# Optimization experiments

Hardware: AMD Instinct MI355X
Metric: run time of the kernel (lower is better)

## Reference

```python
import jax, jax.numpy as jnp
import numpy as np

N, E, F = 32768, 131072, 32

# (l_in, l_edge, l_out, op_type) for each of the 12 active paths; index = row of W
PATHS = [
    (0, 0, 0, 'prod'), (0, 1, 1, 'prod'), (0, 2, 2, 'prod'),
    (1, 0, 1, 'prod'), (2, 0, 2, 'prod'),
    (1, 1, 0, 'dot'), (1, 1, 1, 'cross'), (1, 1, 2, 'outer'),
    (2, 1, 1, 'mat_vec'), (1, 2, 1, 'vec_mat'),
    (2, 2, 0, 'double_dot'), (2, 2, 2, 'mat_mul_sym'),
]


def setup_inputs() -> dict:
    key = jax.random.key(0)
    ks = jax.random.split(key, 8)
    return {
        'h0': jax.random.normal(ks[0], (N, F), jnp.float32),
        'h1': jax.random.normal(ks[1], (N, 3, F), jnp.float32),
        'h2': jax.random.normal(ks[2], (N, 3, 3, F), jnp.float32),
        'g0': jax.random.normal(ks[3], (E, F), jnp.float32),
        'g1': jax.random.normal(ks[4], (E, 3, F), jnp.float32),
        'g2': jax.random.normal(ks[5], (E, 3, 3, F), jnp.float32),
        'W': jax.random.normal(ks[6], (len(PATHS), F, F), jnp.float32) * (F ** -0.5),
        'src': jax.random.randint(ks[7], (E,), 0, N, jnp.int32).astype(jnp.int64),
    }


def _leibniz(h0, h1, h2, g0, g1, g2, W, src):
    inv_sqrt_f = h0.shape[-1] ** -0.5
    # gather source-node features once per l
    h = {0: h0[src], 1: h1[src], 2: h2[src]}
    g = {0: g0, 1: g1, 2: g2}
    eye = jnp.eye(3, dtype=h0.dtype)[None, :, :, None]  # [1,3,3,1]
    msgs = {0: [], 1: [], 2: []}
    for p, (li, le, lo, op) in enumerate(PATHS):
        # nn.Linear(F,F,bias=False): y = x @ W^T, applied on last (feature) axis
        ht = jnp.einsum('...f,gf->...g', h[li], W[p])
        geom = g[le]
        if op == 'prod':
            if li == 0 and le == 0:
                res = ht * geom
            elif li == 0 and le == 1:
                res = ht[:, None, :] * geom
            elif li == 0 and le == 2:
                res = ht[:, None, None, :] * geom
            elif li == 1 and le == 0:
                res = ht * geom[:, None, :]
            else:  # li == 2, le == 0
                res = ht * geom[:, None, None, :]
        elif op == 'dot':
            res = jnp.sum(ht * geom, axis=1)
        elif op == 'cross':
            res = jnp.cross(ht, geom, axisa=1, axisb=1, axisc=1)
        elif op == 'outer':
            outer = ht[:, :, None, :] * geom[:, None, :, :]  # [E,3,3,F]
            trace = jnp.einsum('eiif->ef', outer)
            res = outer - (1.0 / 3.0) * trace[:, None, None, :] * eye
        elif op == 'mat_vec':
            res = jnp.einsum('eijf,ejf->eif', ht, geom)
        elif op == 'vec_mat':
            res = jnp.einsum('eif,eijf->ejf', ht, geom)
        elif op == 'double_dot':
            res = jnp.sum(ht * geom, axis=(1, 2))
        else:  # mat_mul_sym
            raw = jnp.einsum('eikf,ekjf->eijf', ht, geom)
            sym = 0.5 * (raw + jnp.swapaxes(raw, 1, 2))
            trace = jnp.einsum('eiif->ef', sym)
            res = sym - (1.0 / 3.0) * trace[:, None, None, :] * eye
        msgs[lo].append(res * inv_sqrt_f)
    return tuple(sum(msgs[l]) for l in (0, 1, 2))


def reference(h0, h1, h2, g0, g1, g2, W, src):
    return _leibniz(h0, h1, h2, g0, g1, g2, W, src)
```

## Files before the change

kernel.cpp:

```cpp
#include <hip/hip_runtime.h>

typedef float f32x4 __attribute__((ext_vector_type(4)));
typedef __bf16 bf16x8 __attribute__((ext_vector_type(8)));

constexpr float INV_SQRT_F = 0.17677669529663687f;

__device__ __forceinline__ f32x4 mfma16(bf16x8 a, bf16x8 b) {
  const f32x4 z = {0.f, 0.f, 0.f, 0.f};
  return __builtin_amdgcn_mfma_f32_16x16x32_bf16(a, b, z, 0, 0, 0);
}

__device__ __forceinline__ bf16x8 load_frag8(const float* __restrict__ p) {
  f32x4 u = *reinterpret_cast<const f32x4*>(p);
  f32x4 v = *reinterpret_cast<const f32x4*>(p + 4);
  bf16x8 r;
  r[0] = (__bf16)u[0]; r[1] = (__bf16)u[1]; r[2] = (__bf16)u[2]; r[3] = (__bf16)u[3];
  r[4] = (__bf16)v[0]; r[5] = (__bf16)v[1]; r[6] = (__bf16)v[2]; r[7] = (__bf16)v[3];
  return r;
}

__device__ __forceinline__ f32x4 ntload4(const float* __restrict__ p) {
  return __builtin_nontemporal_load(reinterpret_cast<const f32x4*>(p));
}
__device__ __forceinline__ void ntstore4(float* __restrict__ p, f32x4 v) {
  __builtin_nontemporal_store(v, reinterpret_cast<f32x4*>(p));
}

__global__ __launch_bounds__(256, 2)
void leibniz_fused(const float* __restrict__ h0, const float* __restrict__ h1,
                   const float* __restrict__ h2, const float* __restrict__ g0,
                   const float* __restrict__ g1, const float* __restrict__ g2,
                   const float* __restrict__ Wg, const int* __restrict__ src,
                   float* __restrict__ out, int E)
{
  __shared__ bf16x8 wlds[12 * 2 * 4 * 16];

  for (int c = threadIdx.x; c < 12 * 2 * 4 * 16; c += 256) {
    const int gl = c & 15;
    const int qq = (c >> 4) & 3;
    const int hf = (c >> 6) & 1;
    const int p  = c >> 7;
    const float* wp = Wg + (p * 32 + hf * 16 + gl) * 32 + qq * 8;
    bf16x8 f;
#pragma unroll
    for (int j = 0; j < 8; ++j) f[j] = (__bf16)(wp[j] * INV_SQRT_F);
    wlds[c] = f;
  }
  __syncthreads();

  const int lane = threadIdx.x & 63;
  const int wid  = threadIdx.x >> 6;
  const int eidx = lane & 15;
  const int q    = lane >> 4;
  int e0 = (blockIdx.x * 4 + wid) * 16;
  if (e0 > E - 16) e0 = E - 16;

  const int node = src[e0 + eidx];

  const int e   = e0 + eidx;
  const int col = q * 4;
  const float* g0p = g0 + e * 32 + col;
  const float* g1p = g1 + (long long)e * 96 + col;
  const float* g2p = g2 + (long long)e * 288 + col;

  f32x4 gv0[2];
  gv0[0] = ntload4(g0p);
  gv0[1] = ntload4(g0p + 16);
  f32x4 gv1[3][2];
#pragma unroll
  for (int s = 0; s < 3; ++s) {
    gv1[s][0] = ntload4(g1p + s * 32);
    gv1[s][1] = ntload4(g1p + s * 32 + 16);
  }

  const int k0 = q * 8;
  const bf16x8 b0 = load_frag8(h0 + node * 32 + k0);
  bf16x8 b1[3];
#pragma unroll
  for (int s = 0; s < 3; ++s) b1[s] = load_frag8(h1 + node * 96 + s * 32 + k0);
  bf16x8 b2[9];
#pragma unroll
  for (int s = 0; s < 9; ++s) b2[s] = load_frag8(h2 + node * 288 + s * 32 + k0);

  const f32x4 z4 = {0.f, 0.f, 0.f, 0.f};
  f32x4 acc0[2] = {z4, z4};
  f32x4 acc1[3][2];
  f32x4 acc2[9][2];
#pragma unroll
  for (int s = 0; s < 3; ++s) { acc1[s][0] = z4; acc1[s][1] = z4; }
#pragma unroll
  for (int s = 0; s < 9; ++s) { acc2[s][0] = z4; acc2[s][1] = z4; }

#define WFRAG(P, H) (wlds[(((P) * 2 + (H)) * 4 + q) * 16 + eidx])

#pragma unroll
  for (int h = 0; h < 2; ++h) {
    acc0[h] += mfma16(WFRAG(0, h), b0) * gv0[h];
    const bf16x8 w3 = WFRAG(3, h);
#pragma unroll
    for (int s = 0; s < 3; ++s) acc1[s][h] += mfma16(w3, b1[s]) * gv0[h];
    const bf16x8 w4 = WFRAG(4, h);
#pragma unroll
    for (int s = 0; s < 9; ++s) acc2[s][h] += mfma16(w4, b2[s]) * gv0[h];
  }

  f32x4 gkA[3][2];
#pragma unroll
  for (int j = 0; j < 3; ++j) {
    gkA[j][0] = ntload4(g2p + j * 32);
    gkA[j][1] = ntload4(g2p + j * 32 + 16);
  }

#pragma unroll
  for (int h = 0; h < 2; ++h) {
    {
      const f32x4 t = mfma16(WFRAG(1, h), b0);
#pragma unroll
      for (int s = 0; s < 3; ++s) acc1[s][h] += t * gv1[s][h];
    }
    {
      const bf16x8 w5 = WFRAG(5, h);
#pragma unroll
      for (int s = 0; s < 3; ++s) acc0[h] += mfma16(w5, b1[s]) * gv1[s][h];
    }
    {
      const bf16x8 w6 = WFRAG(6, h);
      const f32x4 c0 = mfma16(w6, b1[0]);
      const f32x4 c1 = mfma16(w6, b1[1]);
      const f32x4 c2 = mfma16(w6, b1[2]);
      acc1[0][h] += c1 * gv1[2][h] - c2 * gv1[1][h];
      acc1[1][h] += c2 * gv1[0][h] - c0 * gv1[2][h];
      acc1[2][h] += c0 * gv1[1][h] - c1 * gv1[0][h];
    }
    {
      const bf16x8 w7 = WFRAG(7, h);
      const f32x4 o0 = mfma16(w7, b1[0]);
      const f32x4 o1 = mfma16(w7, b1[1]);
      const f32x4 o2 = mfma16(w7, b1[2]);
      const f32x4 tr3 = (o0 * gv1[0][h] + o1 * gv1[1][h] + o2 * gv1[2][h]) * (1.f / 3.f);
      acc2[0][h] += o0 * gv1[0][h] - tr3;
      acc2[1][h] += o0 * gv1[1][h];
      acc2[2][h] += o0 * gv1[2][h];
      acc2[3][h] += o1 * gv1[0][h];
      acc2[4][h] += o1 * gv1[1][h] - tr3;
      acc2[5][h] += o1 * gv1[2][h];
      acc2[6][h] += o2 * gv1[0][h];
      acc2[7][h] += o2 * gv1[1][h];
      acc2[8][h] += o2 * gv1[2][h] - tr3;
    }
    {
      const bf16x8 w8 = WFRAG(8, h);
#pragma unroll
      for (int i = 0; i < 3; ++i)
#pragma unroll
        for (int j = 0; j < 3; ++j)
          acc1[i][h] += mfma16(w8, b2[i * 3 + j]) * gv1[j][h];
    }
  }

  f32x4 gkB[3][2];
#pragma unroll
  for (int j = 0; j < 3; ++j) {
    gkB[j][0] = ntload4(g2p + (3 + j) * 32);
    gkB[j][1] = ntload4(g2p + (3 + j) * 32 + 16);
  }

  f32x4 t2[2];
  t2[0] = mfma16(WFRAG(2, 0), b0);
  t2[1] = mfma16(WFRAG(2, 1), b0);

#define G2ROW_COMPUTE(K, GK)                                                   \
  {                                                                            \
    _Pragma("unroll")                                                          \
    for (int h = 0; h < 2; ++h) {                                              \
      _Pragma("unroll")                                                        \
      for (int j = 0; j < 3; ++j) acc2[(K) * 3 + j][h] += t2[h] * GK[j][h];    \
      {                                                                        \
        const f32x4 vk = mfma16(WFRAG(9, h), b1[(K)]);                         \
        _Pragma("unroll")                                                      \
        for (int j = 0; j < 3; ++j) acc1[j][h] += vk * GK[j][h];               \
      }                                                                        \
      {                                                                        \
        const bf16x8 w10 = WFRAG(10, h);                                       \
        _Pragma("unroll")                                                      \
        for (int j = 0; j < 3; ++j)                                            \
          acc0[h] += mfma16(w10, b2[(K) * 3 + j]) * GK[j][h];                  \
      }                                                                        \
      {                                                                        \
        const bf16x8 w11 = WFRAG(11, h);                                       \
        const f32x4 m0 = mfma16(w11, b2[0 * 3 + (K)]);                         \
        const f32x4 m1 = mfma16(w11, b2[1 * 3 + (K)]);                         \
        const f32x4 m2 = mfma16(w11, b2[2 * 3 + (K)]);                         \
        const f32x4 tk3 =                                                      \
            (m0 * GK[0][h] + m1 * GK[1][h] + m2 * GK[2][h]) * (1.f / 3.f);     \
        acc2[0][h] += m0 * GK[0][h] - tk3;                                     \
        acc2[4][h] += m1 * GK[1][h] - tk3;                                     \
        acc2[8][h] += m2 * GK[2][h] - tk3;                                     \
        const f32x4 s01 = (m0 * GK[1][h] + m1 * GK[0][h]) * 0.5f;              \
        acc2[1][h] += s01; acc2[3][h] += s01;                                  \
        const f32x4 s02 = (m0 * GK[2][h] + m2 * GK[0][h]) * 0.5f;              \
        acc2[2][h] += s02; acc2[6][h] += s02;                                  \
        const f32x4 s12 = (m1 * GK[2][h] + m2 * GK[1][h]) * 0.5f;              \
        acc2[5][h] += s12; acc2[7][h] += s12;                                  \
      }                                                                        \
    }                                                                          \
  }

  G2ROW_COMPUTE(0, gkA)

#pragma unroll
  for (int j = 0; j < 3; ++j) {
    gkA[j][0] = ntload4(g2p + (6 + j) * 32);
    gkA[j][1] = ntload4(g2p + (6 + j) * 32 + 16);
  }

  G2ROW_COMPUTE(1, gkB)
  G2ROW_COMPUTE(2, gkA)

#undef G2ROW_COMPUTE

  float* o0p = out + (long long)e * 32 + col;
  float* o1p = out + (long long)E * 32 + (long long)e * 96 + col;
  float* o2p = out + (long long)E * 128 + (long long)e * 288 + col;

  ntstore4(o0p, acc0[0]);
  ntstore4(o0p + 16, acc0[1]);
#pragma unroll
  for (int s = 0; s < 3; ++s) {
    ntstore4(o1p + s * 32, acc1[s][0]);
    ntstore4(o1p + s * 32 + 16, acc1[s][1]);
  }
#pragma unroll
  for (int s = 0; s < 9; ++s) {
    ntstore4(o2p + s * 32, acc2[s][0]);
    ntstore4(o2p + s * 32 + 16, acc2[s][1]);
  }
#undef WFRAG
}

extern "C" void kernel_launch(void* const* d_in, const int* in_sizes, int n_in,
                              void* d_out, int out_size, void* d_ws, size_t ws_size,
                              hipStream_t stream) {
  const float* h0 = (const float*)d_in[0];
  const float* h1 = (const float*)d_in[1];
  const float* h2 = (const float*)d_in[2];
  const float* g0 = (const float*)d_in[3];
  const float* g1 = (const float*)d_in[4];
  const float* g2 = (const float*)d_in[5];
  const float* Wg = (const float*)d_in[6];
  const int* src = (const int*)d_in[7];
  const int E = in_sizes[7];
  const int blocks = (E + 63) / 64;
  leibniz_fused<<<blocks, 256, 0, stream>>>(h0, h1, h2, g0, g1, g2, Wg, src,
                                            (float*)d_out, E);
}
```

Measured before the change: 126.9 us.

## Precompute per-node linear transforms into bf16 workspace, then per-edge geometry kernel

Splits the fused kernel into two kernels. The first applies all 12 path weight matrices once per node with MFMA and stores bf16 results in the workspace. The second gathers those per-node transforms for each edge and combines them with the edge geometry using only elementwise math. This removes the redundant per-edge matrix multiplies, but each edge now gathers a larger transformed feature block and there is an extra kernel launch. The original fused kernel is kept as a fallback when the workspace is too small.

After: 198.0 us. +56.1%, slower.

```diff
diff --git a/kernel.cpp b/kernel.cpp
--- a/kernel.cpp
+++ b/kernel.cpp
@@ -2,6 +2,7 @@
 
 typedef float f32x4 __attribute__((ext_vector_type(4)));
 typedef __bf16 bf16x8 __attribute__((ext_vector_type(8)));
+typedef __bf16 bf16x4 __attribute__((ext_vector_type(4)));
 
 constexpr float INV_SQRT_F = 0.17677669529663687f;
 
@@ -9,16 +10,223 @@
   const f32x4 z = {0.f, 0.f, 0.f, 0.f};
   return __builtin_amdgcn_mfma_f32_16x16x32_bf16(a, b, z, 0, 0, 0);
 }
-
-__device__ __forceinline__ bf16x8 load_frag8(const float* __restrict__ p) {
-  f32x4 u = *reinterpret_cast<const f32x4*>(p);
-  f32x4 v = *reinterpret_cast<const f32x4*>(p + 4);
+__device__ __forceinline__ f32x4 ld4(const float* p) {
+  return *reinterpret_cast<const f32x4*>(p);
+}
+__device__ __forceinline__ bf16x4 ldb4(const __bf16* p) {
+  return *reinterpret_cast<const bf16x4*>(p);
+}
+__device__ __forceinline__ f32x4 b2f4(bf16x4 v) {
+  f32x4 r;
+  r[0] = (float)v[0]; r[1] = (float)v[1]; r[2] = (float)v[2]; r[3] = (float)v[3];
+  return r;
+}
+__device__ __forceinline__ bf16x4 f2b4(f32x4 v) {
+  bf16x4 r;
+  r[0] = (__bf16)v[0]; r[1] = (__bf16)v[1]; r[2] = (__bf16)v[2]; r[3] = (__bf16)v[3];
+  return r;
+}
+__device__ __forceinline__ bf16x8 cvt_frag(f32x4 u, f32x4 v) {
   bf16x8 r;
   r[0] = (__bf16)u[0]; r[1] = (__bf16)u[1]; r[2] = (__bf16)u[2]; r[3] = (__bf16)u[3];
   r[4] = (__bf16)v[0]; r[5] = (__bf16)v[1]; r[6] = (__bf16)v[2]; r[7] = (__bf16)v[3];
   return r;
 }
 
+
+__global__ __launch_bounds__(256, 2)
+void node_transform(const float* __restrict__ h0, const float* __restrict__ h1,
+                    const float* __restrict__ h2, const float* __restrict__ Wg,
+                    __bf16* __restrict__ T, int N)
+{
+  __shared__ bf16x8 wlds[12 * 2 * 4 * 16];
+  for (int c = threadIdx.x; c < 12 * 2 * 4 * 16; c += 256) {
+    const int gl = c & 15;
+    const int qq = (c >> 4) & 3;
+    const int hf = (c >> 6) & 1;
+    const int p  = c >> 7;
+    const float* wp = Wg + (p * 32 + hf * 16 + gl) * 32 + qq * 8;
+    bf16x8 f;
+#pragma unroll
+    for (int j = 0; j < 8; ++j) f[j] = (__bf16)(wp[j] * INV_SQRT_F);
+    wlds[c] = f;
+  }
+  __syncthreads();
+
+  const int lane = threadIdx.x & 63;
+  const int wid  = threadIdx.x >> 6;
+  const int eidx = lane & 15;
+  const int q    = lane >> 4;
+  int nb = (blockIdx.x * 4 + wid) * 16;
+  if (nb > N - 16) nb = N - 16;
+  const int node = nb + eidx;
+  const int k0 = q * 8;
+
+  const float* h0p = h0 + (long long)node * 32 + k0;
+  const float* h1p = h1 + (long long)node * 96 + k0;
+  const float* h2p = h2 + (long long)node * 288 + k0;
+  f32x4 r0a = ld4(h0p), r0b = ld4(h0p + 4);
+  f32x4 r1[6];
+#pragma unroll
+  for (int s = 0; s < 3; ++s) { r1[2*s] = ld4(h1p + s*32); r1[2*s+1] = ld4(h1p + s*32 + 4); }
+  f32x4 r2[18];
+#pragma unroll
+  for (int s = 0; s < 9; ++s) { r2[2*s] = ld4(h2p + s*32); r2[2*s+1] = ld4(h2p + s*32 + 4); }
+
+  const bf16x8 b0 = cvt_frag(r0a, r0b);
+  bf16x8 b1[3];
+#pragma unroll
+  for (int s = 0; s < 3; ++s) b1[s] = cvt_frag(r1[2*s], r1[2*s+1]);
+  bf16x8 b2[9];
+#pragma unroll
+  for (int s = 0; s < 9; ++s) b2[s] = cvt_frag(r2[2*s], r2[2*s+1]);
+
+  __bf16* tn = T + (long long)node * 1728;
+
+#define WF(P, H) (wlds[(((P) * 2 + (H)) * 4 + q) * 16 + eidx])
+#define ST(OFF, V) *reinterpret_cast<bf16x4*>(tn + (OFF) + fo) = f2b4(V)
+
+  const int l1p[5] = {3, 5, 6, 7, 9};
+  const int l2p[4] = {4, 8, 10, 11};
+#pragma unroll
+  for (int h = 0; h < 2; ++h) {
+    const int fo = 16 * h + 4 * q;
+    ST(0 * 32, mfma16(WF(0, h), b0));
+    ST(1 * 32, mfma16(WF(1, h), b0));
+    ST(2 * 32, mfma16(WF(2, h), b0));
+#pragma unroll
+    for (int b = 0; b < 5; ++b)
+#pragma unroll
+      for (int s = 0; s < 3; ++s)
+        ST(96 + b * 96 + s * 32, mfma16(WF(l1p[b], h), b1[s]));
+#pragma unroll
+    for (int d = 0; d < 4; ++d)
+#pragma unroll
+      for (int ss = 0; ss < 9; ++ss)
+        ST(576 + d * 288 + ss * 32, mfma16(WF(l2p[d], h), b2[ss]));
+  }
+#undef ST
+#undef WF
+}
+
+__global__ __launch_bounds__(256, 3)
+void edge_geometry(const __bf16* __restrict__ T, const float* __restrict__ g0,
+                   const float* __restrict__ g1, const float* __restrict__ g2,
+                   const int* __restrict__ src, float* __restrict__ out, int E)
+{
+  const int i = blockIdx.x * 256 + threadIdx.x;
+  const int e = i >> 3;
+  if (e >= E) return;
+  const int fo = (i & 7) * 4;
+
+  const int node = src[e];
+  const float* gp0 = g0 + (long long)e * 32 + fo;
+  const float* gp1 = g1 + (long long)e * 96 + fo;
+  const float* gp2 = g2 + (long long)e * 288 + fo;
+  const __bf16* tn = T + (long long)node * 1728 + fo;
+
+  const f32x4 gv0 = ld4(gp0);
+  f32x4 gv1[3];
+#pragma unroll
+  for (int s = 0; s < 3; ++s) gv1[s] = ld4(gp1 + s * 32);
+  f32x4 gkA[3], gkB[3];
+#pragma unroll
+  for (int j = 0; j < 3; ++j) gkA[j] = ld4(gp2 + j * 32);
+#pragma unroll
+  for (int j = 0; j < 3; ++j) gkB[j] = ld4(gp2 + (3 + j) * 32);
+
+  f32x4 acc0 = b2f4(ldb4(tn + 0)) * gv0;
+  f32x4 acc1[3];
+#pragma unroll
+  for (int s = 0; s < 3; ++s) acc1[s] = b2f4(ldb4(tn + 96 + s * 32)) * gv0;
+  f32x4 acc2[9];
+#pragma unroll
+  for (int ss = 0; ss < 9; ++ss) acc2[ss] = b2f4(ldb4(tn + 576 + ss * 32)) * gv0;
+
+  {
+    const f32x4 h1v = b2f4(ldb4(tn + 32));
+#pragma unroll
+    for (int s = 0; s < 3; ++s) acc1[s] += h1v * gv1[s];
+  }
+#pragma unroll
+  for (int s = 0; s < 3; ++s)
+    acc0 += b2f4(ldb4(tn + 192 + s * 32)) * gv1[s];
+  {
+    f32x4 h6[3];
+#pragma unroll
+    for (int s = 0; s < 3; ++s) h6[s] = b2f4(ldb4(tn + 288 + s * 32));
+    acc1[0] += h6[1] * gv1[2] - h6[2] * gv1[1];
+    acc1[1] += h6[2] * gv1[0] - h6[0] * gv1[2];
+    acc1[2] += h6[0] * gv1[1] - h6[1] * gv1[0];
+  }
+  {
+    f32x4 h7[3];
+#pragma unroll
+    for (int s = 0; s < 3; ++s) h7[s] = b2f4(ldb4(tn + 384 + s * 32));
+    const f32x4 tr3 = (h7[0] * gv1[0] + h7[1] * gv1[1] + h7[2] * gv1[2]) * (1.f / 3.f);
+#pragma unroll
+    for (int a = 0; a < 3; ++a)
+#pragma unroll
+      for (int b = 0; b < 3; ++b) acc2[a * 3 + b] += h7[a] * gv1[b];
+    acc2[0] -= tr3; acc2[4] -= tr3; acc2[8] -= tr3;
+  }
+#pragma unroll
+  for (int a = 0; a < 3; ++a)
+#pragma unroll
+    for (int b = 0; b < 3; ++b)
+      acc1[a] += b2f4(ldb4(tn + 864 + (a * 3 + b) * 32)) * gv1[b];
+
+  const f32x4 h2v = b2f4(ldb4(tn + 64));
+  f32x4 h9[3];
+#pragma unroll
+  for (int s = 0; s < 3; ++s) h9[s] = b2f4(ldb4(tn + 480 + s * 32));
+
+#define G2ROW(K, GK)                                                           \
+  {                                                                            \
+    _Pragma("unroll")                                                          \
+    for (int j = 0; j < 3; ++j) acc2[(K) * 3 + j] += h2v * GK[j];              \
+    _Pragma("unroll")                                                          \
+    for (int j = 0; j < 3; ++j) acc1[j] += h9[(K)] * GK[j];                    \
+    _Pragma("unroll")                                                          \
+    for (int j = 0; j < 3; ++j)                                                \
+      acc0 += b2f4(ldb4(tn + 1152 + ((K) * 3 + j) * 32)) * GK[j];              \
+    {                                                                          \
+      const f32x4 m0 = b2f4(ldb4(tn + 1440 + (0 * 3 + (K)) * 32));             \
+      const f32x4 m1 = b2f4(ldb4(tn + 1440 + (1 * 3 + (K)) * 32));             \
+      const f32x4 m2 = b2f4(ldb4(tn + 1440 + (2 * 3 + (K)) * 32));             \
+      const f32x4 tk3 = (m0 * GK[0] + m1 * GK[1] + m2 * GK[2]) * (1.f / 3.f);  \
+      acc2[0] += m0 * GK[0] - tk3;                                             \
+      acc2[4] += m1 * GK[1] - tk3;                                             \
+      acc2[8] += m2 * GK[2] - tk3;                                             \
+      const f32x4 s01 = (m0 * GK[1] + m1 * GK[0]) * 0.5f;                      \
+      acc2[1] += s01; acc2[3] += s01;                                          \
+      const f32x4 s02 = (m0 * GK[2] + m2 * GK[0]) * 0.5f;                      \
+      acc2[2] += s02; acc2[6] += s02;                                          \
+      const f32x4 s12 = (m1 * GK[2] + m2 * GK[1]) * 0.5f;                      \
+      acc2[5] += s12; acc2[7] += s12;                                          \
+    }                                                                          \
+  }
+
+  G2ROW(0, gkA)
+#pragma unroll
+  for (int j = 0; j < 3; ++j) gkA[j] = ld4(gp2 + (6 + j) * 32);
+  G2ROW(1, gkB)
+  G2ROW(2, gkA)
+#undef G2ROW
+
+  float* o0p = out + (long long)e * 32 + fo;
+  float* o1p = out + (long long)E * 32 + (long long)e * 96 + fo;
+  float* o2p = out + (long long)E * 128 + (long long)e * 288 + fo;
+  *reinterpret_cast<f32x4*>(o0p) = acc0;
+#pragma unroll
+  for (int s = 0; s < 3; ++s) *reinterpret_cast<f32x4*>(o1p + s * 32) = acc1[s];
+#pragma unroll
+  for (int s = 0; s < 9; ++s) *reinterpret_cast<f32x4*>(o2p + s * 32) = acc2[s];
+}
+
+__device__ __forceinline__ bf16x8 load_frag8(const float* __restrict__ p) {
+  return cvt_frag(ld4(p), ld4(p + 4));
+}
 __device__ __forceinline__ f32x4 ntload4(const float* __restrict__ p) {
   return __builtin_nontemporal_load(reinterpret_cast<const f32x4*>(p));
 }
@@ -34,7 +242,6 @@
                    float* __restrict__ out, int E)
 {
   __shared__ bf16x8 wlds[12 * 2 * 4 * 16];
-
   for (int c = threadIdx.x; c < 12 * 2 * 4 * 16; c += 256) {
     const int gl = c & 15;
     const int qq = (c >> 4) & 3;
@@ -56,7 +263,6 @@
   if (e0 > E - 16) e0 = E - 16;
 
   const int node = src[e0 + eidx];
-
   const int e   = e0 + eidx;
   const int col = q * 4;
   const float* g0p = g0 + e * 32 + col;
@@ -64,8 +270,7 @@
   const float* g2p = g2 + (long long)e * 288 + col;
 
   f32x4 gv0[2];
-  gv0[0] = ntload4(g0p);
-  gv0[1] = ntload4(g0p + 16);
+  gv0[0] = ntload4(g0p); gv0[1] = ntload4(g0p + 16);
   f32x4 gv1[3][2];
 #pragma unroll
   for (int s = 0; s < 3; ++s) {
@@ -92,7 +297,6 @@
   for (int s = 0; s < 9; ++s) { acc2[s][0] = z4; acc2[s][1] = z4; }
 
 #define WFRAG(P, H) (wlds[(((P) * 2 + (H)) * 4 + q) * 16 + eidx])
-
 #pragma unroll
   for (int h = 0; h < 2; ++h) {
     acc0[h] += mfma16(WFRAG(0, h), b0) * gv0[h];
@@ -151,10 +355,10 @@
     {
       const bf16x8 w8 = WFRAG(8, h);
 #pragma unroll
-      for (int i = 0; i < 3; ++i)
-#pragma unroll
-        for (int j = 0; j < 3; ++j)
-          acc1[i][h] += mfma16(w8, b2[i * 3 + j]) * gv1[j][h];
+      for (int a = 0; a < 3; ++a)
+#pragma unroll
+        for (int b = 0; b < 3; ++b)
+          acc1[a][h] += mfma16(w8, b2[a * 3 + b]) * gv1[b][h];
     }
   }
 
@@ -207,22 +411,18 @@
   }
 
   G2ROW_COMPUTE(0, gkA)
-
 #pragma unroll
   for (int j = 0; j < 3; ++j) {
     gkA[j][0] = ntload4(g2p + (6 + j) * 32);
     gkA[j][1] = ntload4(g2p + (6 + j) * 32 + 16);
   }
-
   G2ROW_COMPUTE(1, gkB)
   G2ROW_COMPUTE(2, gkA)
-
 #undef G2ROW_COMPUTE
 
   float* o0p = out + (long long)e * 32 + col;
   float* o1p = out + (long long)E * 32 + (long long)e * 96 + col;
   float* o2p = out + (long long)E * 128 + (long long)e * 288 + col;
-
   ntstore4(o0p, acc0[0]);
   ntstore4(o0p + 16, acc0[1]);
 #pragma unroll
@@ -250,7 +450,16 @@
   const float* Wg = (const float*)d_in[6];
   const int* src = (const int*)d_in[7];
   const int E = in_sizes[7];
-  const int blocks = (E + 63) / 64;
-  leibniz_fused<<<blocks, 256, 0, stream>>>(h0, h1, h2, g0, g1, g2, Wg, src,
-                                            (float*)d_out, E);
-}
+  const int N = in_sizes[0] / 32;
+
+  const size_t need = (size_t)N * 1728 * 2;
+  if (ws_size >= need) {
+    __bf16* T = (__bf16*)d_ws;
+    node_transform<<<(N + 63) / 64, 256, 0, stream>>>(h0, h1, h2, Wg, T, N);
+    edge_geometry<<<(E * 8 + 255) / 256, 256, 0, stream>>>(T, g0, g1, g2, src,
+                                                           (float*)d_out, E);
+  } else {
+    leibniz_fused<<<(E + 63) / 64, 256, 0, stream>>>(h0, h1, h2, g0, g1, g2,
+                                                     Wg, src, (float*)d_out, E);
+  }
+}
```

## Add bf16 prepass for node features and split feature halves across waves

Applied to the files above, without the earlier changes.

Adds a prepass kernel that converts h0/h1/h2 and the scaled W to bf16 in workspace, so the main kernel gathers half-size node rows instead of fp32 rows it converts per edge. The main kernel now gives each wave one 16-column half of the outputs, which halves per-thread accumulators and register pressure and loads all of g2 up front. It also switches from nontemporal to regular loads and stores. The cost is an extra launch plus a full read and write pass over the node features, and each weight tile is now fetched from workspace per block.

New measurement: 141.1 us. +11.2%, slower.

```diff
diff --git a/kernel.cpp b/kernel.cpp
--- a/kernel.cpp
+++ b/kernel.cpp
@@ -2,6 +2,7 @@
 
 typedef float f32x4 __attribute__((ext_vector_type(4)));
 typedef __bf16 bf16x8 __attribute__((ext_vector_type(8)));
+typedef __bf16 bf16x4 __attribute__((ext_vector_type(4)));
 
 constexpr float INV_SQRT_F = 0.17677669529663687f;
 
@@ -9,16 +10,222 @@
   const f32x4 z = {0.f, 0.f, 0.f, 0.f};
   return __builtin_amdgcn_mfma_f32_16x16x32_bf16(a, b, z, 0, 0, 0);
 }
-
-__device__ __forceinline__ bf16x8 load_frag8(const float* __restrict__ p) {
-  f32x4 u = *reinterpret_cast<const f32x4*>(p);
-  f32x4 v = *reinterpret_cast<const f32x4*>(p + 4);
+__device__ __forceinline__ f32x4 ld4(const float* p) {
+  return *reinterpret_cast<const f32x4*>(p);
+}
+__device__ __forceinline__ bf16x8 ldb8(const __bf16* __restrict__ p) {
+  return *reinterpret_cast<const bf16x8*>(p);
+}
+__device__ __forceinline__ bf16x8 cvt_frag(f32x4 u, f32x4 v) {
   bf16x8 r;
   r[0] = (__bf16)u[0]; r[1] = (__bf16)u[1]; r[2] = (__bf16)u[2]; r[3] = (__bf16)u[3];
   r[4] = (__bf16)v[0]; r[5] = (__bf16)v[1]; r[6] = (__bf16)v[2]; r[7] = (__bf16)v[3];
   return r;
 }
 
+__global__ __launch_bounds__(256)
+void leibniz_prepass(const float* __restrict__ h0, const float* __restrict__ h1,
+                     const float* __restrict__ h2, const float* __restrict__ Wg,
+                     __bf16* __restrict__ ws, int n0, int n1, int n2)
+{
+  if (blockIdx.x == 0) {
+    bf16x8* wsW = reinterpret_cast<bf16x8*>(ws);
+    for (int c = threadIdx.x; c < 12 * 2 * 4 * 16; c += 256) {
+      const int gl = c & 15;
+      const int qq = (c >> 4) & 3;
+      const int hf = (c >> 6) & 1;
+      const int p  = c >> 7;
+      const float* wp = Wg + (p * 32 + hf * 16 + gl) * 32 + qq * 8;
+      bf16x8 f;
+#pragma unroll
+      for (int j = 0; j < 8; ++j) f[j] = (__bf16)(wp[j] * INV_SQRT_F);
+      wsW[c] = f;
+    }
+  }
+  __bf16* hb0 = ws + 12288;
+  __bf16* hb1 = hb0 + n0;
+  __bf16* hb2 = hb1 + n1;
+  const int q0 = n0 >> 2, q1 = n1 >> 2, q2 = n2 >> 2;
+  const int total = q0 + q1 + q2;
+  for (int i = blockIdx.x * 256 + threadIdx.x; i < total; i += gridDim.x * 256) {
+    const float* sp;
+    __bf16* dp;
+    if (i < q0)           { sp = h0 + 4 * i;              dp = hb0 + 4 * i; }
+    else if (i < q0 + q1) { int j = i - q0;      sp = h1 + 4 * j; dp = hb1 + 4 * j; }
+    else                  { int j = i - q0 - q1; sp = h2 + 4 * j; dp = hb2 + 4 * j; }
+    const f32x4 v = *reinterpret_cast<const f32x4*>(sp);
+    bf16x4 o;
+    o[0] = (__bf16)v[0]; o[1] = (__bf16)v[1]; o[2] = (__bf16)v[2]; o[3] = (__bf16)v[3];
+    *reinterpret_cast<bf16x4*>(dp) = o;
+  }
+}
+
+__global__ __launch_bounds__(256, 2)
+void leibniz_half(const __bf16* __restrict__ wsAll,
+                  const float* __restrict__ g0, const float* __restrict__ g1,
+                  const float* __restrict__ g2, const int* __restrict__ src,
+                  float* __restrict__ out, int E, int n0, int n1)
+{
+  __shared__ bf16x8 wlds[12 * 2 * 4 * 16];
+  {
+    const bf16x8* wsW = reinterpret_cast<const bf16x8*>(wsAll);
+    for (int c = threadIdx.x; c < 12 * 2 * 4 * 16; c += 256) wlds[c] = wsW[c];
+  }
+  __syncthreads();
+
+  const __bf16* hb0 = wsAll + 12288;
+  const __bf16* hb1 = hb0 + n0;
+  const __bf16* hb2 = hb1 + n1;
+
+  const int lane = threadIdx.x & 63;
+  const int wid  = threadIdx.x >> 6;
+  const int half = wid & 1;
+  const int tile = wid >> 1;
+  const int eidx = lane & 15;
+  const int q    = lane >> 4;
+  int e0 = (blockIdx.x * 2 + tile) * 16;
+  if (e0 > E - 16) e0 = E - 16;
+
+  const int node = src[e0 + eidx];
+  const int e    = e0 + eidx;
+  const int col  = q * 4 + 16 * half;
+
+  const float* g0p = g0 + (long long)e * 32 + col;
+  const float* g1p = g1 + (long long)e * 96 + col;
+  const float* g2p = g2 + (long long)e * 288 + col;
+  const f32x4 gv0 = ld4(g0p);
+  f32x4 gv1[3];
+#pragma unroll
+  for (int s = 0; s < 3; ++s) gv1[s] = ld4(g1p + s * 32);
+  f32x4 gk[9];
+#pragma unroll
+  for (int s = 0; s < 9; ++s) gk[s] = ld4(g2p + s * 32);
+
+  const int k0 = q * 8;
+  const bf16x8 b0 = ldb8(hb0 + (long long)node * 32 + k0);
+  bf16x8 b1[3];
+#pragma unroll
+  for (int s = 0; s < 3; ++s) b1[s] = ldb8(hb1 + (long long)node * 96 + s * 32 + k0);
+  bf16x8 b2[9];
+#pragma unroll
+  for (int s = 0; s < 9; ++s) b2[s] = ldb8(hb2 + (long long)node * 288 + s * 32 + k0);
+
+#define WFRAG(P) (wlds[(((P) * 2 + half) * 4 + q) * 16 + eidx])
+
+  f32x4 acc0 = mfma16(WFRAG(0), b0) * gv0;
+  f32x4 acc1[3];
+  f32x4 acc2[9];
+  {
+    const bf16x8 w3 = WFRAG(3);
+#pragma unroll
+    for (int s = 0; s < 3; ++s) acc1[s] = mfma16(w3, b1[s]) * gv0;
+    const bf16x8 w4 = WFRAG(4);
+#pragma unroll
+    for (int s = 0; s < 9; ++s) acc2[s] = mfma16(w4, b2[s]) * gv0;
+  }
+
+  {
+    const f32x4 t = mfma16(WFRAG(1), b0);
+#pragma unroll
+    for (int s = 0; s < 3; ++s) acc1[s] += t * gv1[s];
+  }
+  {
+    const bf16x8 w5 = WFRAG(5);
+#pragma unroll
+    for (int s = 0; s < 3; ++s) acc0 += mfma16(w5, b1[s]) * gv1[s];
+  }
+  {
+    const bf16x8 w6 = WFRAG(6);
+    const f32x4 c0 = mfma16(w6, b1[0]);
+    const f32x4 c1 = mfma16(w6, b1[1]);
+    const f32x4 c2 = mfma16(w6, b1[2]);
+    acc1[0] += c1 * gv1[2] - c2 * gv1[1];
+    acc1[1] += c2 * gv1[0] - c0 * gv1[2];
+    acc1[2] += c0 * gv1[1] - c1 * gv1[0];
+  }
+  {
+    const bf16x8 w7 = WFRAG(7);
+    const f32x4 o0 = mfma16(w7, b1[0]);
+    const f32x4 o1 = mfma16(w7, b1[1]);
+    const f32x4 o2 = mfma16(w7, b1[2]);
+    const f32x4 tr3 = (o0 * gv1[0] + o1 * gv1[1] + o2 * gv1[2]) * (1.f / 3.f);
+    acc2[0] += o0 * gv1[0] - tr3;
+    acc2[1] += o0 * gv1[1];
+    acc2[2] += o0 * gv1[2];
+    acc2[3] += o1 * gv1[0];
+    acc2[4] += o1 * gv1[1] - tr3;
+    acc2[5] += o1 * gv1[2];
+    acc2[6] += o2 * gv1[0];
+    acc2[7] += o2 * gv1[1];
+    acc2[8] += o2 * gv1[2] - tr3;
+  }
+  {
+    const bf16x8 w8 = WFRAG(8);
+#pragma unroll
+    for (int a = 0; a < 3; ++a)
+#pragma unroll
+      for (int b = 0; b < 3; ++b)
+        acc1[a] += mfma16(w8, b2[a * 3 + b]) * gv1[b];
+  }
+
+  {
+    const f32x4 t2 = mfma16(WFRAG(2), b0);
+#pragma unroll
+    for (int ss = 0; ss < 9; ++ss) acc2[ss] += t2 * gk[ss];
+  }
+  {
+    const bf16x8 w9 = WFRAG(9);
+#pragma unroll
+    for (int i = 0; i < 3; ++i) {
+      const f32x4 vk = mfma16(w9, b1[i]);
+#pragma unroll
+      for (int j = 0; j < 3; ++j) acc1[j] += vk * gk[i * 3 + j];
+    }
+  }
+  {
+    const bf16x8 w10 = WFRAG(10);
+#pragma unroll
+    for (int ss = 0; ss < 9; ++ss) acc0 += mfma16(w10, b2[ss]) * gk[ss];
+  }
+  {
+    const bf16x8 w11 = WFRAG(11);
+#pragma unroll
+    for (int k = 0; k < 3; ++k) {
+      const f32x4 m0 = mfma16(w11, b2[0 * 3 + k]);
+      const f32x4 m1 = mfma16(w11, b2[1 * 3 + k]);
+      const f32x4 m2 = mfma16(w11, b2[2 * 3 + k]);
+      const f32x4 gk0 = gk[k * 3 + 0];
+      const f32x4 gk1 = gk[k * 3 + 1];
+      const f32x4 gk2 = gk[k * 3 + 2];
+      const f32x4 tk3 = (m0 * gk0 + m1 * gk1 + m2 * gk2) * (1.f / 3.f);
+      acc2[0] += m0 * gk0 - tk3;
+      acc2[4] += m1 * gk1 - tk3;
+      acc2[8] += m2 * gk2 - tk3;
+      const f32x4 s01 = (m0 * gk1 + m1 * gk0) * 0.5f;
+      acc2[1] += s01; acc2[3] += s01;
+      const f32x4 s02 = (m0 * gk2 + m2 * gk0) * 0.5f;
+      acc2[2] += s02; acc2[6] += s02;
+      const f32x4 s12 = (m1 * gk2 + m2 * gk1) * 0.5f;
+      acc2[5] += s12; acc2[7] += s12;
+    }
+  }
+
+  __builtin_amdgcn_s_barrier();
+
+  float* o0p = out + (long long)e * 32 + col;
+  float* o1p = out + (long long)E * 32 + (long long)e * 96 + col;
+  float* o2p = out + (long long)E * 128 + (long long)e * 288 + col;
+  *reinterpret_cast<f32x4*>(o0p) = acc0;
+#pragma unroll
+  for (int s = 0; s < 3; ++s) *reinterpret_cast<f32x4*>(o1p + s * 32) = acc1[s];
+#pragma unroll
+  for (int s = 0; s < 9; ++s) *reinterpret_cast<f32x4*>(o2p + s * 32) = acc2[s];
+#undef WFRAG
+}
+
+__device__ __forceinline__ bf16x8 load_frag8(const float* __restrict__ p) {
+  return cvt_frag(ld4(p), ld4(p + 4));
+}
 __device__ __forceinline__ f32x4 ntload4(const float* __restrict__ p) {
   return __builtin_nontemporal_load(reinterpret_cast<const f32x4*>(p));
 }
@@ -34,7 +241,6 @@
                    float* __restrict__ out, int E)
 {
   __shared__ bf16x8 wlds[12 * 2 * 4 * 16];
-
   for (int c = threadIdx.x; c < 12 * 2 * 4 * 16; c += 256) {
     const int gl = c & 15;
     const int qq = (c >> 4) & 3;
@@ -56,7 +262,6 @@
   if (e0 > E - 16) e0 = E - 16;
 
   const int node = src[e0 + eidx];
-
   const int e   = e0 + eidx;
   const int col = q * 4;
   const float* g0p = g0 + e * 32 + col;
@@ -64,8 +269,7 @@
   const float* g2p = g2 + (long long)e * 288 + col;
 
   f32x4 gv0[2];
-  gv0[0] = ntload4(g0p);
-  gv0[1] = ntload4(g0p + 16);
+  gv0[0] = ntload4(g0p); gv0[1] = ntload4(g0p + 16);
   f32x4 gv1[3][2];
 #pragma unroll
   for (int s = 0; s < 3; ++s) {
@@ -92,7 +296,6 @@
   for (int s = 0; s < 9; ++s) { acc2[s][0] = z4; acc2[s][1] = z4; }
 
 #define WFRAG(P, H) (wlds[(((P) * 2 + (H)) * 4 + q) * 16 + eidx])
-
 #pragma unroll
   for (int h = 0; h < 2; ++h) {
     acc0[h] += mfma16(WFRAG(0, h), b0) * gv0[h];
@@ -151,10 +354,10 @@
     {
       const bf16x8 w8 = WFRAG(8, h);
 #pragma unroll
-      for (int i = 0; i < 3; ++i)
-#pragma unroll
-        for (int j = 0; j < 3; ++j)
-          acc1[i][h] += mfma16(w8, b2[i * 3 + j]) * gv1[j][h];
+      for (int a = 0; a < 3; ++a)
+#pragma unroll
+        for (int b = 0; b < 3; ++b)
+          acc1[a][h] += mfma16(w8, b2[a * 3 + b]) * gv1[b][h];
     }
   }
 
@@ -207,22 +410,18 @@
   }
 
   G2ROW_COMPUTE(0, gkA)
-
 #pragma unroll
   for (int j = 0; j < 3; ++j) {
     gkA[j][0] = ntload4(g2p + (6 + j) * 32);
     gkA[j][1] = ntload4(g2p + (6 + j) * 32 + 16);
   }
-
   G2ROW_COMPUTE(1, gkB)
   G2ROW_COMPUTE(2, gkA)
-
 #undef G2ROW_COMPUTE
 
   float* o0p = out + (long long)e * 32 + col;
   float* o1p = out + (long long)E * 32 + (long long)e * 96 + col;
   float* o2p = out + (long long)E * 128 + (long long)e * 288 + col;
-
   ntstore4(o0p, acc0[0]);
   ntstore4(o0p + 16, acc0[1]);
 #pragma unroll
@@ -250,7 +449,16 @@
   const float* Wg = (const float*)d_in[6];
   const int* src = (const int*)d_in[7];
   const int E = in_sizes[7];
-  const int blocks = (E + 63) / 64;
-  leibniz_fused<<<blocks, 256, 0, stream>>>(h0, h1, h2, g0, g1, g2, Wg, src,
-                                            (float*)d_out, E);
-}
+  const int n0 = in_sizes[0], n1 = in_sizes[1], n2 = in_sizes[2];
+
+  const size_t need = 24576 + (size_t)(n0 + n1 + n2) * 2;
+  if (ws_size >= need) {
+    __bf16* ws = (__bf16*)d_ws;
+    leibniz_prepass<<<2048, 256, 0, stream>>>(h0, h1, h2, Wg, ws, n0, n1, n2);
+    leibniz_half<<<(E + 31) / 32, 256, 0, stream>>>(ws, g0, g1, g2, src,
+                                                    (float*)d_out, E, n0, n1);
+  } else {
+    leibniz_fused<<<(E + 63) / 64, 256, 0, stream>>>(h0, h1, h2, g0, g1, g2,
+                                                     Wg, src, (float*)d_out, E);
+  }
+}
```

## Add bf16 prepass and persistent double-buffered DMA-to-LDS main kernel

Applied to the files above, without the earlier changes.

Adds a prepass kernel that converts W (scaled) and node features h0/h1/h2 to bf16 in the workspace, which halves the gathered bytes per edge. The main kernel becomes persistent over 16-edge tiles and uses global_load_lds to stage g0/g1/g2 into double-buffered LDS while the node features for the next tile are prefetched into registers, so loads overlap compute. W fragments stay in registers. In exchange there is an extra launch and a full pass over the node arrays, plus heavier register pressure from keeping two sets of h fragments live.

Measured after the change: 171.3 us. 35.0% more time.

```diff
diff --git a/kernel.cpp b/kernel.cpp
--- a/kernel.cpp
+++ b/kernel.cpp
@@ -2,6 +2,7 @@
 
 typedef float f32x4 __attribute__((ext_vector_type(4)));
 typedef __bf16 bf16x8 __attribute__((ext_vector_type(8)));
+typedef __bf16 bf16x4 __attribute__((ext_vector_type(4)));
 
 constexpr float INV_SQRT_F = 0.17677669529663687f;
 
@@ -9,16 +10,267 @@
   const f32x4 z = {0.f, 0.f, 0.f, 0.f};
   return __builtin_amdgcn_mfma_f32_16x16x32_bf16(a, b, z, 0, 0, 0);
 }
-
-__device__ __forceinline__ bf16x8 load_frag8(const float* __restrict__ p) {
-  f32x4 u = *reinterpret_cast<const f32x4*>(p);
-  f32x4 v = *reinterpret_cast<const f32x4*>(p + 4);
+__device__ __forceinline__ f32x4 ld4(const float* p) {
+  return *reinterpret_cast<const f32x4*>(p);
+}
+__device__ __forceinline__ bf16x8 ldb8(const __bf16* __restrict__ p) {
+  return *reinterpret_cast<const bf16x8*>(p);
+}
+__device__ __forceinline__ bf16x8 cvt_frag(f32x4 u, f32x4 v) {
   bf16x8 r;
   r[0] = (__bf16)u[0]; r[1] = (__bf16)u[1]; r[2] = (__bf16)u[2]; r[3] = (__bf16)u[3];
   r[4] = (__bf16)v[0]; r[5] = (__bf16)v[1]; r[6] = (__bf16)v[2]; r[7] = (__bf16)v[3];
   return r;
 }
-
+__device__ __forceinline__ void stage16(const float* gp, float* lp) {
+  __builtin_amdgcn_global_load_lds(
+      (const __attribute__((address_space(1))) void*)gp,
+      (__attribute__((address_space(3))) void*)lp, 16, 0, 0);
+}
+
+__global__ __launch_bounds__(256)
+void leibniz_prepass(const float* __restrict__ h0, const float* __restrict__ h1,
+                     const float* __restrict__ h2, const float* __restrict__ Wg,
+                     __bf16* __restrict__ ws, int n0, int n1, int n2)
+{
+  if (blockIdx.x == 0) {
+    bf16x8* wsW = reinterpret_cast<bf16x8*>(ws);
+    for (int c = threadIdx.x; c < 12 * 2 * 4 * 16; c += 256) {
+      const int gl = c & 15;
+      const int qq = (c >> 4) & 3;
+      const int hf = (c >> 6) & 1;
+      const int p  = c >> 7;
+      const float* wp = Wg + (p * 32 + hf * 16 + gl) * 32 + qq * 8;
+      bf16x8 f;
+#pragma unroll
+      for (int j = 0; j < 8; ++j) f[j] = (__bf16)(wp[j] * INV_SQRT_F);
+      wsW[c] = f;
+    }
+  }
+  __bf16* hb0 = ws + 12288;
+  __bf16* hb1 = hb0 + n0;
+  __bf16* hb2 = hb1 + n1;
+  const int q0 = n0 >> 2, q1 = n1 >> 2, q2 = n2 >> 2;
+  const int total = q0 + q1 + q2;
+  for (int i = blockIdx.x * 256 + threadIdx.x; i < total; i += gridDim.x * 256) {
+    const float* sp;
+    __bf16* dp;
+    if (i < q0)           { sp = h0 + 4 * i;              dp = hb0 + 4 * i; }
+    else if (i < q0 + q1) { int j = i - q0;      sp = h1 + 4 * j; dp = hb1 + 4 * j; }
+    else                  { int j = i - q0 - q1; sp = h2 + 4 * j; dp = hb2 + 4 * j; }
+    const f32x4 v = *reinterpret_cast<const f32x4*>(sp);
+    bf16x4 o;
+    o[0] = (__bf16)v[0]; o[1] = (__bf16)v[1]; o[2] = (__bf16)v[2]; o[3] = (__bf16)v[3];
+    *reinterpret_cast<bf16x4*>(dp) = o;
+  }
+}
+
+__global__ __launch_bounds__(128, 2)
+void leibniz_dma(const __bf16* __restrict__ wsAll,
+                 const float* __restrict__ g0, const float* __restrict__ g1,
+                 const float* __restrict__ g2, const int* __restrict__ src,
+                 float* __restrict__ out, int E, int n0, int n1)
+{
+  __shared__ __align__(16) float smem[4 * 3328];
+
+  const int lane = threadIdx.x & 63;
+  const int half = threadIdx.x >> 6;
+  const int eidx = lane & 15;
+  const int q    = lane >> 4;
+
+  bf16x8 w[12];
+  {
+    const bf16x8* wsW = reinterpret_cast<const bf16x8*>(wsAll);
+#pragma unroll
+    for (int p = 0; p < 12; ++p) w[p] = wsW[(p * 2 + half) * 64 + q * 16 + eidx];
+  }
+  const __bf16* hb0 = wsAll + 12288;
+  const __bf16* hb1 = hb0 + n0;
+  const __bf16* hb2 = hb1 + n1;
+
+  const int NT  = (E + 15) >> 4;
+  const int NBg = gridDim.x;
+  const long long o1base = (long long)E * 32;
+  const long long o2base = (long long)E * 128;
+  const int col = q * 4 + 16 * half;
+
+#define EBASE(T) ((long long)(T) * 16 > (long long)E - 16 ? (long long)E - 16 \
+                                                          : (long long)(T) * 16)
+
+#define STAGE(TILE, BUF) do {                                                  \
+  const long long eb_ = EBASE(TILE);                                           \
+  float* lb_ = smem + (half * 2 + (BUF)) * 3328;                               \
+  const float* s0_ = g0 + (eb_ + eidx) * 32 + col;                             \
+  stage16(s0_, lb_);                                                           \
+  const float* s1_ = g1 + (eb_ + eidx) * 96 + col;                             \
+  _Pragma("unroll")                                                            \
+  for (int s = 0; s < 3; ++s) stage16(s1_ + s * 32, lb_ + (1 + s) * 256);      \
+  const float* s2_ = g2 + (eb_ + eidx) * 288 + col;                            \
+  _Pragma("unroll")                                                            \
+  for (int ss = 0; ss < 9; ++ss) stage16(s2_ + ss * 32, lb_ + (4 + ss) * 256); \
+} while (0)
+
+#define LOAD_H(NODE, B0, B1, B2) do {                                          \
+  const __bf16* p0_ = hb0 + (long long)(NODE) * 32 + q * 8;                    \
+  B0 = ldb8(p0_);                                                              \
+  const __bf16* p1_ = hb1 + (long long)(NODE) * 96 + q * 8;                    \
+  _Pragma("unroll") for (int s = 0; s < 3; ++s) B1[s] = ldb8(p1_ + s * 32);    \
+  const __bf16* p2_ = hb2 + (long long)(NODE) * 288 + q * 8;                   \
+  _Pragma("unroll") for (int s = 0; s < 9; ++s) B2[s] = ldb8(p2_ + s * 32);    \
+} while (0)
+
+#define COMPUTE_STORE(TILE, CUR, B0, B1, B2) do {                              \
+  const long long e_ = EBASE(TILE) + eidx;                                     \
+  const float* lb = smem + (half * 2 + (CUR)) * 3328 + lane * 4;               \
+                      \
+  const f32x4 gv0 = ld4(lb);                                                   \
+  f32x4 acc0 = mfma16(w[0], B0) * gv0;                                         \
+  f32x4 acc1[3];                                                               \
+  f32x4 acc2[9];                                                               \
+  {                                                                            \
+    _Pragma("unroll")                                                          \
+    for (int s = 0; s < 3; ++s) acc1[s] = mfma16(w[3], B1[s]) * gv0;           \
+    _Pragma("unroll")                                                          \
+    for (int s = 0; s < 9; ++s) acc2[s] = mfma16(w[4], B2[s]) * gv0;           \
+  }                                                                            \
+                                                \
+  {                                                                            \
+    f32x4 gv1[3];                                                              \
+    _Pragma("unroll")                                                          \
+    for (int s = 0; s < 3; ++s) gv1[s] = ld4(lb + (1 + s) * 256);              \
+    {                                                                          \
+      const f32x4 t = mfma16(w[1], B0);                                        \
+      _Pragma("unroll")                                                        \
+      for (int s = 0; s < 3; ++s) acc1[s] += t * gv1[s];                       \
+    }                                                                          \
+    _Pragma("unroll")                                                          \
+    for (int s = 0; s < 3; ++s) acc0 += mfma16(w[5], B1[s]) * gv1[s];          \
+    {                                                                          \
+      const f32x4 c0 = mfma16(w[6], B1[0]);                                    \
+      const f32x4 c1 = mfma16(w[6], B1[1]);                                    \
+      const f32x4 c2 = mfma16(w[6], B1[2]);                                    \
+      acc1[0] += c1 * gv1[2] - c2 * gv1[1];                                    \
+      acc1[1] += c2 * gv1[0] - c0 * gv1[2];                                    \
+      acc1[2] += c0 * gv1[1] - c1 * gv1[0];                                    \
+    }                                                                          \
+    {                                                                          \
+      const f32x4 o0 = mfma16(w[7], B1[0]);                                    \
+      const f32x4 o1 = mfma16(w[7], B1[1]);                                    \
+      const f32x4 o2 = mfma16(w[7], B1[2]);                                    \
+      const f32x4 tr3 =                                                        \
+          (o0 * gv1[0] + o1 * gv1[1] + o2 * gv1[2]) * (1.f / 3.f);             \
+      acc2[0] += o0 * gv1[0] - tr3;                                            \
+      acc2[1] += o0 * gv1[1];                                                  \
+      acc2[2] += o0 * gv1[2];                                                  \
+      acc2[3] += o1 * gv1[0];                                                  \
+      acc2[4] += o1 * gv1[1] - tr3;                                            \
+      acc2[5] += o1 * gv1[2];                                                  \
+      acc2[6] += o2 * gv1[0];                                                  \
+      acc2[7] += o2 * gv1[1];                                                  \
+      acc2[8] += o2 * gv1[2] - tr3;                                            \
+    }                                                                          \
+    _Pragma("unroll")                                                          \
+    for (int a = 0; a < 3; ++a)                                                \
+      _Pragma("unroll")                                                        \
+      for (int b = 0; b < 3; ++b)                                              \
+        acc1[a] += mfma16(w[8], B2[a * 3 + b]) * gv1[b];                       \
+  }                                                                            \
+            \
+  {                                                                            \
+    const f32x4 t2 = mfma16(w[2], B0);                                         \
+    _Pragma("unroll")                                                          \
+    for (int k = 0; k < 3; ++k) {                                              \
+      f32x4 gk[3];                                                             \
+      _Pragma("unroll")                                                        \
+      for (int j = 0; j < 3; ++j) gk[j] = ld4(lb + (4 + k * 3 + j) * 256);     \
+      _Pragma("unroll")                                                        \
+      for (int j = 0; j < 3; ++j) acc2[k * 3 + j] += t2 * gk[j];               \
+      {                                                                        \
+        const f32x4 vk = mfma16(w[9], B1[k]);                                  \
+        _Pragma("unroll")                                                      \
+        for (int j = 0; j < 3; ++j) acc1[j] += vk * gk[j];                     \
+      }                                                                        \
+      _Pragma("unroll")                                                        \
+      for (int j = 0; j < 3; ++j)                                              \
+        acc0 += mfma16(w[10], B2[k * 3 + j]) * gk[j];                          \
+      {                                                                        \
+        const f32x4 m0 = mfma16(w[11], B2[0 * 3 + k]);                         \
+        const f32x4 m1 = mfma16(w[11], B2[1 * 3 + k]);                         \
+        const f32x4 m2 = mfma16(w[11], B2[2 * 3 + k]);                         \
+        const f32x4 tk3 = (m0 * gk[0] + m1 * gk[1] + m2 * gk[2]) * (1.f/3.f);  \
+        acc2[0] += m0 * gk[0] - tk3;                                           \
+        acc2[4] += m1 * gk[1] - tk3;                                           \
+        acc2[8] += m2 * gk[2] - tk3;                                           \
+        const f32x4 s01 = (m0 * gk[1] + m1 * gk[0]) * 0.5f;                    \
+        acc2[1] += s01; acc2[3] += s01;                                        \
+        const f32x4 s02 = (m0 * gk[2] + m2 * gk[0]) * 0.5f;                    \
+        acc2[2] += s02; acc2[6] += s02;                                        \
+        const f32x4 s12 = (m1 * gk[2] + m2 * gk[1]) * 0.5f;                    \
+        acc2[5] += s12; acc2[7] += s12;                                        \
+      }                                                                        \
+    }                                                                          \
+  }                                                                            \
+         \
+  {                                                                            \
+    float* o0p = out + e_ * 32 + col;                                          \
+    float* o1p = out + o1base + e_ * 96 + col;                                 \
+    float* o2p = out + o2base + e_ * 288 + col;                                \
+    *reinterpret_cast<f32x4*>(o0p) = acc0;                                     \
+    _Pragma("unroll")                                                          \
+    for (int s = 0; s < 3; ++s)                                                \
+      *reinterpret_cast<f32x4*>(o1p + s * 32) = acc1[s];                       \
+    _Pragma("unroll")                                                          \
+    for (int s = 0; s < 9; ++s)                                                \
+      *reinterpret_cast<f32x4*>(o2p + s * 32) = acc2[s];                       \
+  }                                                                            \
+} while (0)
+
+  int tile = blockIdx.x;
+  if (tile >= NT) return;
+
+  const int nodeA0 = src[EBASE(tile) + eidx];
+  STAGE(tile, 0);
+  bf16x8 bA0, bA1[3], bA2[9];
+  bf16x8 bB0, bB1[3], bB2[9];
+  LOAD_H(nodeA0, bA0, bA1, bA2);
+  int nnext = 0;
+  if (tile + NBg < NT) nnext = src[EBASE(tile + NBg) + eidx];
+  int cur = 0;
+
+#define ITER(BC0, BC1, BC2, BN0, BN1, BN2)                                     \
+  {                                                                            \
+    asm volatile("s_waitcnt vmcnt(0)" ::: "memory");                           \
+    __builtin_amdgcn_sched_barrier(0);                                         \
+    __builtin_amdgcn_s_barrier();                    \
+    const int tn_ = tile + NBg;                                                \
+    const bool hn_ = tn_ < NT;                                                 \
+    if (hn_) {                                                                 \
+      STAGE(tn_, cur ^ 1);                                                     \
+      LOAD_H(nnext, BN0, BN1, BN2);                                            \
+      const int t2_ = tile + 2 * NBg;                                          \
+      if (t2_ < NT) nnext = src[EBASE(t2_) + eidx];                            \
+    }                                                                          \
+    COMPUTE_STORE(tile, cur, BC0, BC1, BC2);                                   \
+    if (!hn_) break;                                                           \
+    tile = tn_;                                                                \
+    cur ^= 1;                                                                  \
+  }
+
+  for (;;) {
+    ITER(bA0, bA1, bA2, bB0, bB1, bB2)
+    ITER(bB0, bB1, bB2, bA0, bA1, bA2)
+  }
+
+#undef ITER
+#undef COMPUTE_STORE
+#undef LOAD_H
+#undef STAGE
+#undef EBASE
+}
+
+__device__ __forceinline__ bf16x8 load_frag8(const float* __restrict__ p) {
+  return cvt_frag(ld4(p), ld4(p + 4));
+}
 __device__ __forceinline__ f32x4 ntload4(const float* __restrict__ p) {
   return __builtin_nontemporal_load(reinterpret_cast<const f32x4*>(p));
 }
@@ -34,7 +286,6 @@
                    float* __restrict__ out, int E)
 {
   __shared__ bf16x8 wlds[12 * 2 * 4 * 16];
-
   for (int c = threadIdx.x; c < 12 * 2 * 4 * 16; c += 256) {
     const int gl = c & 15;
     const int qq = (c >> 4) & 3;
@@ -56,7 +307,6 @@
   if (e0 > E - 16) e0 = E - 16;
 
   const int node = src[e0 + eidx];
-
   const int e   = e0 + eidx;
   const int col = q * 4;
   const float* g0p = g0 + e * 32 + col;
@@ -64,8 +314,7 @@
   const float* g2p = g2 + (long long)e * 288 + col;
 
   f32x4 gv0[2];
-  gv0[0] = ntload4(g0p);
-  gv0[1] = ntload4(g0p + 16);
+  gv0[0] = ntload4(g0p); gv0[1] = ntload4(g0p + 16);
   f32x4 gv1[3][2];
 #pragma unroll
   for (int s = 0; s < 3; ++s) {
@@ -92,7 +341,6 @@
   for (int s = 0; s < 9; ++s) { acc2[s][0] = z4; acc2[s][1] = z4; }
 
 #define WFRAG(P, H) (wlds[(((P) * 2 + (H)) * 4 + q) * 16 + eidx])
-
 #pragma unroll
   for (int h = 0; h < 2; ++h) {
     acc0[h] += mfma16(WFRAG(0, h), b0) * gv0[h];
@@ -151,10 +399,10 @@
     {
       const bf16x8 w8 = WFRAG(8, h);
 #pragma unroll
-      for (int i = 0; i < 3; ++i)
-#pragma unroll
-        for (int j = 0; j < 3; ++j)
-          acc1[i][h] += mfma16(w8, b2[i * 3 + j]) * gv1[j][h];
+      for (int a = 0; a < 3; ++a)
+#pragma unroll
+        for (int b = 0; b < 3; ++b)
+          acc1[a][h] += mfma16(w8, b2[a * 3 + b]) * gv1[b][h];
     }
   }
 
@@ -207,22 +455,18 @@
   }
 
   G2ROW_COMPUTE(0, gkA)
-
 #pragma unroll
   for (int j = 0; j < 3; ++j) {
     gkA[j][0] = ntload4(g2p + (6 + j) * 32);
     gkA[j][1] = ntload4(g2p + (6 + j) * 32 + 16);
   }
-
   G2ROW_COMPUTE(1, gkB)
   G2ROW_COMPUTE(2, gkA)
-
 #undef G2ROW_COMPUTE
 
   float* o0p = out + (long long)e * 32 + col;
   float* o1p = out + (long long)E * 32 + (long long)e * 96 + col;
   float* o2p = out + (long long)E * 128 + (long long)e * 288 + col;
-
   ntstore4(o0p, acc0[0]);
   ntstore4(o0p + 16, acc0[1]);
 #pragma unroll
@@ -250,7 +494,19 @@
   const float* Wg = (const float*)d_in[6];
   const int* src = (const int*)d_in[7];
   const int E = in_sizes[7];
-  const int blocks = (E + 63) / 64;
-  leibniz_fused<<<blocks, 256, 0, stream>>>(h0, h1, h2, g0, g1, g2, Wg, src,
-                                            (float*)d_out, E);
-}
+  const int n0 = in_sizes[0], n1 = in_sizes[1], n2 = in_sizes[2];
+
+  const size_t need = 24576 + (size_t)(n0 + n1 + n2) * 2;
+  if (ws_size >= need) {
+    __bf16* ws = (__bf16*)d_ws;
+    leibniz_prepass<<<2048, 256, 0, stream>>>(h0, h1, h2, Wg, ws, n0, n1, n2);
+    const int NT = (E + 15) / 16;
+    int blocks = 768;
+    if (blocks > NT) blocks = NT;
+    leibniz_dma<<<blocks, 128, 0, stream>>>(ws, g0, g1, g2, src,
+                                            (float*)d_out, E, n0, n1);
+  } else {
+    leibniz_fused<<<(E + 63) / 64, 256, 0, stream>>>(h0, h1, h2, g0, g1, g2,
+                                                     Wg, src, (float*)d_out, E);
+  }
+}
```
